# Kernel tuning notes

Hardware: AMD Instinct MI355X
Metric: run time of the kernel (lower is better)

Reference implementation:

```python
import jax, jax.numpy as jnp
import numpy as np

N_HEADS = 12
C = 3          # per-head in/hidden/out channels (12/4)
C_PRED = 1     # predictor hidden (4/4)
BN_EPS = 1e-5
COS_EPS = 1e-8
B, H, W = 8, 512, 768


def setup_inputs() -> dict:
    key = jax.random.key(0)
    ks = jax.random.split(key, 22)
    p = lambda k, s: jax.random.normal(k, s, jnp.float32) * 0.1
    return {
        "latent1": jax.random.normal(ks[0], (B, N_HEADS, H, W), jnp.float32),
        "latent2": jax.random.normal(ks[1], (B, N_HEADS, H, W), jnp.float32),
        # projector conv1 + BN
        "W1": p(ks[2], (N_HEADS, C, C)), "b1": p(ks[3], (N_HEADS, C)),
        "g1": 1.0 + p(ks[4], (N_HEADS, C)), "be1": p(ks[5], (N_HEADS, C)),
        # projector conv2 + BN
        "W2": p(ks[6], (N_HEADS, C, C)), "b2": p(ks[7], (N_HEADS, C)),
        "g2": 1.0 + p(ks[8], (N_HEADS, C)), "be2": p(ks[9], (N_HEADS, C)),
        # projector conv3 + BN (no ReLU)
        "W3": p(ks[10], (N_HEADS, C, C)), "b3": p(ks[11], (N_HEADS, C)),
        "g3": 1.0 + p(ks[12], (N_HEADS, C)), "be3": p(ks[13], (N_HEADS, C)),
        # predictor conv1 + BN
        "W4": p(ks[14], (N_HEADS, C_PRED, C)), "b4": p(ks[15], (N_HEADS, C_PRED)),
        "g4": 1.0 + p(ks[16], (N_HEADS, C_PRED)), "be4": p(ks[17], (N_HEADS, C_PRED)),
        # predictor conv2 (no BN)
        "W5": p(ks[18], (N_HEADS, C, C_PRED)), "b5": p(ks[19], (N_HEADS, C)),
    }


def _conv1x1(x, Wk, bk):
    # x: [B, Cin, H, W'], Wk: [Cout, Cin]
    return jnp.einsum('oc,bchw->bohw', Wk, x) + bk[None, :, None, None]


def _bn(x, g, be):
    # training-mode BatchNorm2d: batch statistics over (B, H, W)
    m = x.mean(axis=(0, 2, 3), keepdims=True)
    v = x.var(axis=(0, 2, 3), keepdims=True)  # biased var, as torch BN uses
    return (x - m) * jax.lax.rsqrt(v + BN_EPS) * g[None, :, None, None] + be[None, :, None, None]


def _cos_loss(p, z):
    # -mean(cosine_similarity(p, detach(z), dim=1))
    z = jax.lax.stop_gradient(z)
    dot = jnp.sum(p * z, axis=1)
    npn = jnp.maximum(jnp.sqrt(jnp.sum(p * p, axis=1)), COS_EPS)
    nzn = jnp.maximum(jnp.sqrt(jnp.sum(z * z, axis=1)), COS_EPS)
    return -jnp.mean(dot / (npn * nzn))


def _head_loss(x1, x2, W1, b1, g1, be1, W2, b2, g2, be2, W3, b3, g3, be3,
               W4, b4, g4, be4, W5, b5):
    def proj(x):
        x = jax.nn.relu(_bn(_conv1x1(x, W1, b1), g1, be1))
        x = jax.nn.relu(_bn(_conv1x1(x, W2, b2), g2, be2))
        return _bn(_conv1x1(x, W3, b3), g3, be3)

    def pred(z):
        h = jax.nn.relu(_bn(_conv1x1(z, W4, b4), g4, be4))
        return _conv1x1(h, W5, b5)

    z1, z2 = proj(x1), proj(x2)
    p1, p2 = pred(z1), pred(z2)
    return 0.5 * (_cos_loss(p1, z2) + _cos_loss(p2, z1))


def reference(latent1, latent2, W1, b1, g1, be1, W2, b2, g2, be2,
              W3, b3, g3, be3, W4, b4, g4, be4, W5, b5):
    Bd, Cd, Hd, Wd = latent1.shape
    Wp = Wd // C
    # per-channel view [B, H, W] -> [B, 3, H, W/3]; stack heads on leading axis
    x1 = latent1.reshape(Bd, N_HEADS, C, Hd, Wp).transpose(1, 0, 2, 3, 4)
    x2 = latent2.reshape(Bd, N_HEADS, C, Hd, Wp).transpose(1, 0, 2, 3, 4)
    losses = jax.vmap(_head_loss)(x1, x2, W1, b1, g1, be1, W2, b2, g2, be2,
                                  W3, b3, g3, be3, W4, b4, g4, be4, W5, b5)
    return jnp.sum(losses)
```

## Files before the change

kernel.cpp:

```cpp
#include <hip/hip_runtime.h>
#include <math.h>


typedef unsigned short ushort_t;
typedef unsigned int uint_t;

constexpr int   NH      = 12;
constexpr int   POS     = 131072;
constexpr int   NB      = 8;
constexpr long long MLL = (long long)NB * POS;
constexpr int   CSPAN   = POS / 16;
constexpr int   SBLK    = 128;
constexpr int   NTOT    = NB * NH * 3 * POS;
constexpr float COS_EPS = 1e-8f;

constexpr size_t XB_BYTES   = (size_t)NTOT * 2;
constexpr size_t DBL_COUNT  = (size_t)24 * SBLK * 9 + (size_t)24 * SBLK * 6 +
                              (size_t)24 * SBLK * 9 + (size_t)12 * SBLK;
constexpr size_t NEED_BYTES = 2 * XB_BYTES + DBL_COUNT * 8 + 480 * 4;

template <int K>
__device__ inline void block_reduce_to0(double (&v)[K]) {
#pragma unroll
  for (int off = 32; off > 0; off >>= 1) {
#pragma unroll
    for (int k = 0; k < K; ++k) v[k] += __shfl_down(v[k], off, 64);
  }
  __shared__ double lds[4][K];
  const int lane = threadIdx.x & 63;
  const int wv   = threadIdx.x >> 6;
  if (lane == 0) {
#pragma unroll
    for (int k = 0; k < K; ++k) lds[wv][k] = v[k];
  }
  __syncthreads();
  if (threadIdx.x == 0) {
#pragma unroll
    for (int k = 0; k < K; ++k) v[k] = lds[0][k] + lds[1][k] + lds[2][k] + lds[3][k];
  }
}

__device__ inline uint_t pack2bf(float lo, float hi) {
  uint_t ul = __float_as_uint(lo);
  uint_t uh = __float_as_uint(hi);
  ul = ul + 0x7FFFu + ((ul >> 16) & 1u);
  uh = uh + 0x7FFFu + ((uh >> 16) & 1u);
  return (ul >> 16) | (uh & 0xFFFF0000u);
}

__device__ inline void unpack8(const uint4 v, float (&f)[8]) {
  const uint_t w0 = v.x, w1 = v.y, w2 = v.z, w3 = v.w;
  f[0] = __uint_as_float(w0 << 16); f[1] = __uint_as_float(w0 & 0xFFFF0000u);
  f[2] = __uint_as_float(w1 << 16); f[3] = __uint_as_float(w1 & 0xFFFF0000u);
  f[4] = __uint_as_float(w2 << 16); f[5] = __uint_as_float(w2 & 0xFFFF0000u);
  f[6] = __uint_as_float(w3 << 16); f[7] = __uint_as_float(w3 & 0xFFFF0000u);
}

template <bool BF16>
__device__ inline void load_ch3(const float* __restrict__ X,
                                const ushort_t* __restrict__ XB,
                                size_t eoff, float (&f)[3][8]) {
#pragma unroll
  for (int c = 0; c < 3; ++c) {
    const size_t a = eoff + (size_t)c * POS;
    if constexpr (BF16) {
      const uint4 v = *(const uint4*)(XB + a);
      unpack8(v, f[c]);
    } else {
      const float4 u0 = *(const float4*)(X + a);
      const float4 u1 = *(const float4*)(X + a + 4);
      f[c][0] = u0.x; f[c][1] = u0.y; f[c][2] = u0.z; f[c][3] = u0.w;
      f[c][4] = u1.x; f[c][5] = u1.y; f[c][6] = u1.z; f[c][7] = u1.w;
    }
  }
}

template <bool STORE>
__global__ __launch_bounds__(256) void passA_kernel(
    const float* __restrict__ x1, const float* __restrict__ x2,
    ushort_t* __restrict__ xb1, ushort_t* __restrict__ xb2,
    double* __restrict__ P0) {
  const int u = blockIdx.y;
  const int s = u % 24;
  const int b = u / 24;
  const int n = s >> 1;
  const float* __restrict__ X = (s & 1) ? x2 : x1;
  ushort_t* __restrict__ XB = (s & 1) ? xb2 : xb1;
  const size_t off0 = (size_t)((b * NH + n) * 3) * POS + (size_t)blockIdx.x * CSPAN;

  float acc[9] = {0.f, 0.f, 0.f, 0.f, 0.f, 0.f, 0.f, 0.f, 0.f};
#pragma unroll
  for (int i = 0; i < 8; ++i) {
    const int idx = i * 1024 + threadIdx.x * 4;
    float4 v[3];
#pragma unroll
    for (int c = 0; c < 3; ++c)
      v[c] = *(const float4*)(X + off0 + (size_t)c * POS + idx);
    if constexpr (STORE) {
#pragma unroll
      for (int c = 0; c < 3; ++c) {
        uint2 h;
        h.x = pack2bf(v[c].x, v[c].y);
        h.y = pack2bf(v[c].z, v[c].w);
        *(uint2*)(XB + off0 + (size_t)c * POS + idx) = h;
      }
    }
    const float* f0 = (const float*)&v[0];
    const float* f1 = (const float*)&v[1];
    const float* f2 = (const float*)&v[2];
#pragma unroll
    for (int j = 0; j < 4; ++j) {
      const float X0 = f0[j], X1 = f1[j], X2 = f2[j];
      acc[0] += X0;      acc[1] += X1;      acc[2] += X2;
      acc[3] += X0 * X0; acc[4] += X1 * X1; acc[5] += X2 * X2;
      acc[6] += X0 * X1; acc[7] += X0 * X2; acc[8] += X1 * X2;
    }
  }

  double v9[9];
#pragma unroll
  for (int k = 0; k < 9; ++k) v9[k] = (double)acc[k];
  block_reduce_to0<9>(v9);
  if (threadIdx.x == 0) {
    double* dst = P0 + ((size_t)s * SBLK + b * 16 + blockIdx.x) * 9;
#pragma unroll
    for (int k = 0; k < 9; ++k) dst[k] = v9[k];
  }
}

__global__ __launch_bounds__(256) void bn_statsA_kernel(
    const double* __restrict__ P0, const float* __restrict__ W1,
    const float* __restrict__ b1, const float* __restrict__ g1,
    const float* __restrict__ be1, float* __restrict__ derived) {
  const int s = blockIdx.x;
  const int t = threadIdx.x;
  const int n = s >> 1;
  double v[9] = {0, 0, 0, 0, 0, 0, 0, 0, 0};
  if (t < SBLK) {
    const double* p = P0 + ((size_t)s * SBLK + t) * 9;
#pragma unroll
    for (int k = 0; k < 9; ++k) v[k] = p[k];
  }
  block_reduce_to0<9>(v);
  if (t == 0) {
    const double M = (double)MLL;
    double m[3] = {v[0] / M, v[1] / M, v[2] / M};
    double C00 = v[3] / M - m[0] * m[0];
    double C11 = v[4] / M - m[1] * m[1];
    double C22 = v[5] / M - m[2] * m[2];
    double C01 = v[6] / M - m[0] * m[1];
    double C02 = v[7] / M - m[0] * m[2];
    double C12 = v[8] / M - m[1] * m[2];
    for (int o = 0; o < 3; ++o) {
      const double w0 = W1[n * 9 + o * 3 + 0];
      const double w1v = W1[n * 9 + o * 3 + 1];
      const double w2v = W1[n * 9 + o * 3 + 2];
      const double my = w0 * m[0] + w1v * m[1] + w2v * m[2] + (double)b1[n * 3 + o];
      const double vy = w0 * w0 * C00 + w1v * w1v * C11 + w2v * w2v * C22 +
                        2.0 * (w0 * w1v * C01 + w0 * w2v * C02 + w1v * w2v * C12);
      const double sc = (double)g1[n * 3 + o] / sqrt(vy + 1e-5);
      derived[s * 20 + o]     = (float)sc;
      derived[s * 20 + 3 + o] = (float)((double)be1[n * 3 + o] - my * sc);
    }
  }
}

template <bool BF16>
__global__ __launch_bounds__(256) void passB_kernel(
    const float* __restrict__ x1, const float* __restrict__ x2,
    const ushort_t* __restrict__ xb1, const ushort_t* __restrict__ xb2,
    const float* __restrict__ W1, const float* __restrict__ b1,
    const float* __restrict__ W2, const float* __restrict__ b2,
    const float* __restrict__ derived, double* __restrict__ P2) {
  const int u = blockIdx.y;
  const int s = u % 24;
  const int b = u / 24;
  const int n = s >> 1;
  const float* __restrict__ X = (s & 1) ? x2 : x1;
  const ushort_t* __restrict__ XB = (s & 1) ? xb2 : xb1;
  const size_t off0 = (size_t)((b * NH + n) * 3) * POS + (size_t)blockIdx.x * CSPAN;

  float w1[3][3], bb1[3], w2[3][3], bb2[3], s1[3], t1[3];
#pragma unroll
  for (int o = 0; o < 3; ++o) {
#pragma unroll
    for (int c = 0; c < 3; ++c) {
      w1[o][c] = W1[n * 9 + o * 3 + c];
      w2[o][c] = W2[n * 9 + o * 3 + c];
    }
    bb1[o] = b1[n * 3 + o];
    bb2[o] = b2[n * 3 + o];
    s1[o]  = derived[s * 20 + o];
    t1[o]  = derived[s * 20 + 3 + o];
  }

  float acc[6] = {0.f, 0.f, 0.f, 0.f, 0.f, 0.f};
#pragma unroll 2
  for (int i = 0; i < 4; ++i) {
    const size_t eoff = off0 + i * 2048 + threadIdx.x * 8;
    float f[3][8];
    load_ch3<BF16>(X, XB, eoff, f);
#pragma unroll
    for (int j = 0; j < 8; ++j) {
      const float X0 = f[0][j], X1 = f[1][j], X2 = f[2][j];
      float a[3];
#pragma unroll
      for (int o = 0; o < 3; ++o) {
        const float y = fmaf(w1[o][0], X0, fmaf(w1[o][1], X1, fmaf(w1[o][2], X2, bb1[o])));
        a[o] = fmaxf(0.f, fmaf(s1[o], y, t1[o]));
      }
#pragma unroll
      for (int o = 0; o < 3; ++o) {
        const float y2v = fmaf(w2[o][0], a[0], fmaf(w2[o][1], a[1], fmaf(w2[o][2], a[2], bb2[o])));
        acc[o]     += y2v;
        acc[3 + o] += y2v * y2v;
      }
    }
  }

  double v[6];
#pragma unroll
  for (int k = 0; k < 6; ++k) v[k] = (double)acc[k];
  block_reduce_to0<6>(v);
  if (threadIdx.x == 0) {
    double* dst = P2 + ((size_t)s * SBLK + b * 16 + blockIdx.x) * 6;
#pragma unroll
    for (int k = 0; k < 6; ++k) dst[k] = v[k];
  }
}

__global__ __launch_bounds__(256) void bn_statsB_kernel(
    const double* __restrict__ P2, const float* __restrict__ gamma,
    const float* __restrict__ beta, float* __restrict__ derived) {
  const int s = blockIdx.x;
  const int t = threadIdx.x;
  const int n = s >> 1;
  double v[6] = {0, 0, 0, 0, 0, 0};
  if (t < SBLK) {
    const double* p = P2 + ((size_t)s * SBLK + t) * 6;
#pragma unroll
    for (int k = 0; k < 6; ++k) v[k] = p[k];
  }
  block_reduce_to0<6>(v);
  if (t == 0) {
#pragma unroll
    for (int c = 0; c < 3; ++c) {
      const double mean = v[c] / (double)MLL;
      const double var  = v[3 + c] / (double)MLL - mean * mean;
      const double sc   = (double)gamma[n * 3 + c] / sqrt(var + 1e-5);
      derived[s * 20 + 6 + c] = (float)sc;
      derived[s * 20 + 9 + c] = (float)((double)beta[n * 3 + c] - mean * sc);
    }
  }
}

template <bool BF16>
__global__ __launch_bounds__(256) void passC_kernel(
    const float* __restrict__ x1, const float* __restrict__ x2,
    const ushort_t* __restrict__ xb1, const ushort_t* __restrict__ xb2,
    const float* __restrict__ W1, const float* __restrict__ b1,
    const float* __restrict__ W2, const float* __restrict__ b2,
    const float* __restrict__ W3, const float* __restrict__ b3,
    const float* __restrict__ derived, double* __restrict__ P3) {
  const int u = blockIdx.y;
  const int s = u % 24;
  const int b = u / 24;
  const int n = s >> 1;
  const float* __restrict__ X = (s & 1) ? x2 : x1;
  const ushort_t* __restrict__ XB = (s & 1) ? xb2 : xb1;
  const size_t off0 = (size_t)((b * NH + n) * 3) * POS + (size_t)blockIdx.x * CSPAN;

  float w1[3][3], bb1[3], w2[3][3], bb2[3], w3[3][3], bb3[3];
  float s1[3], t1[3], s2[3], t2[3];
#pragma unroll
  for (int o = 0; o < 3; ++o) {
#pragma unroll
    for (int c = 0; c < 3; ++c) {
      w1[o][c] = W1[n * 9 + o * 3 + c];
      w2[o][c] = W2[n * 9 + o * 3 + c];
      w3[o][c] = W3[n * 9 + o * 3 + c];
    }
    bb1[o] = b1[n * 3 + o];
    bb2[o] = b2[n * 3 + o];
    bb3[o] = b3[n * 3 + o];
    s1[o]  = derived[s * 20 + o];
    t1[o]  = derived[s * 20 + 3 + o];
    s2[o]  = derived[s * 20 + 6 + o];
    t2[o]  = derived[s * 20 + 9 + o];
  }

  float acc[9] = {0.f, 0.f, 0.f, 0.f, 0.f, 0.f, 0.f, 0.f, 0.f};
#pragma unroll 2
  for (int i = 0; i < 4; ++i) {
    const size_t eoff = off0 + i * 2048 + threadIdx.x * 8;
    float f[3][8];
    load_ch3<BF16>(X, XB, eoff, f);
#pragma unroll
    for (int j = 0; j < 8; ++j) {
      const float X0 = f[0][j], X1 = f[1][j], X2 = f[2][j];
      float a[3], a2[3], y3[3];
#pragma unroll
      for (int o = 0; o < 3; ++o) {
        const float y = fmaf(w1[o][0], X0, fmaf(w1[o][1], X1, fmaf(w1[o][2], X2, bb1[o])));
        a[o] = fmaxf(0.f, fmaf(s1[o], y, t1[o]));
      }
#pragma unroll
      for (int o = 0; o < 3; ++o) {
        const float y = fmaf(w2[o][0], a[0], fmaf(w2[o][1], a[1], fmaf(w2[o][2], a[2], bb2[o])));
        a2[o] = fmaxf(0.f, fmaf(s2[o], y, t2[o]));
      }
#pragma unroll
      for (int o = 0; o < 3; ++o) {
        y3[o] = fmaf(w3[o][0], a2[0], fmaf(w3[o][1], a2[1], fmaf(w3[o][2], a2[2], bb3[o])));
        acc[o]     += y3[o];
        acc[3 + o] += y3[o] * y3[o];
      }
      acc[6] += y3[0] * y3[1];
      acc[7] += y3[0] * y3[2];
      acc[8] += y3[1] * y3[2];
    }
  }

  double v[9];
#pragma unroll
  for (int k = 0; k < 9; ++k) v[k] = (double)acc[k];
  block_reduce_to0<9>(v);
  if (threadIdx.x == 0) {
    double* dst = P3 + ((size_t)s * SBLK + b * 16 + blockIdx.x) * 9;
#pragma unroll
    for (int k = 0; k < 9; ++k) dst[k] = v[k];
  }
}

__global__ __launch_bounds__(256) void bn_statsC_kernel(
    const double* __restrict__ P3, const float* __restrict__ g3,
    const float* __restrict__ be3, const float* __restrict__ W4,
    const float* __restrict__ b4, const float* __restrict__ g4,
    const float* __restrict__ be4, float* __restrict__ derived) {
  const int s = blockIdx.x;
  const int t = threadIdx.x;
  const int n = s >> 1;
  double v[9] = {0, 0, 0, 0, 0, 0, 0, 0, 0};
  if (t < SBLK) {
    const double* p = P3 + ((size_t)s * SBLK + t) * 9;
#pragma unroll
    for (int k = 0; k < 9; ++k) v[k] = p[k];
  }
  block_reduce_to0<9>(v);
  if (t == 0) {
    const double M = (double)MLL;
    double mean[3] = {v[0] / M, v[1] / M, v[2] / M};
    double cov[3][3];
    cov[0][0] = v[3] / M - mean[0] * mean[0];
    cov[1][1] = v[4] / M - mean[1] * mean[1];
    cov[2][2] = v[5] / M - mean[2] * mean[2];
    cov[0][1] = cov[1][0] = v[6] / M - mean[0] * mean[1];
    cov[0][2] = cov[2][0] = v[7] / M - mean[0] * mean[2];
    cov[1][2] = cov[2][1] = v[8] / M - mean[1] * mean[2];

    double s3[3], t3[3];
    for (int c = 0; c < 3; ++c) {
      s3[c] = (double)g3[n * 3 + c] / sqrt(cov[c][c] + 1e-5);
      t3[c] = (double)be3[n * 3 + c] - mean[c] * s3[c];
      derived[s * 20 + 12 + c] = (float)s3[c];
      derived[s * 20 + 15 + c] = (float)t3[c];
    }
    double u[3], dd = (double)b4[n];
    for (int c = 0; c < 3; ++c) {
      u[c] = (double)W4[n * 3 + c] * s3[c];
      dd += (double)W4[n * 3 + c] * t3[c];
    }
    double m4 = dd;
    for (int c = 0; c < 3; ++c) m4 += u[c] * mean[c];
    double v4 = 0.0;
    for (int i = 0; i < 3; ++i)
      for (int j = 0; j < 3; ++j) v4 += u[i] * u[j] * cov[i][j];
    const double s4 = (double)g4[n] / sqrt(v4 + 1e-5);
    derived[s * 20 + 18] = (float)s4;
    derived[s * 20 + 19] = (float)((double)be4[n] - m4 * s4);
  }
}

__device__ inline void fwd_chain(
    const float w1[3][3], const float bb1[3],
    const float w2[3][3], const float bb2[3],
    const float w3[3][3], const float bb3[3],
    const float w4[3], float b4s, const float w5[3], const float b5v[3],
    const float* S, float X0, float X1, float X2, float z[3], float p[3]) {
  float a[3], a2[3];
#pragma unroll
  for (int o = 0; o < 3; ++o) {
    const float y = fmaf(w1[o][0], X0, fmaf(w1[o][1], X1, fmaf(w1[o][2], X2, bb1[o])));
    a[o] = fmaxf(0.f, fmaf(S[o], y, S[3 + o]));
  }
#pragma unroll
  for (int o = 0; o < 3; ++o) {
    const float y = fmaf(w2[o][0], a[0], fmaf(w2[o][1], a[1], fmaf(w2[o][2], a[2], bb2[o])));
    a2[o] = fmaxf(0.f, fmaf(S[6 + o], y, S[9 + o]));
  }
  float y4 = b4s;
#pragma unroll
  for (int o = 0; o < 3; ++o) {
    const float y = fmaf(w3[o][0], a2[0], fmaf(w3[o][1], a2[1], fmaf(w3[o][2], a2[2], bb3[o])));
    z[o] = fmaf(S[12 + o], y, S[15 + o]);
    y4 = fmaf(w4[o], z[o], y4);
  }
  const float h = fmaxf(0.f, fmaf(S[18], y4, S[19]));
#pragma unroll
  for (int o = 0; o < 3; ++o) p[o] = fmaf(w5[o], h, b5v[o]);
}

template <bool BF16>
__global__ __launch_bounds__(256) void passD_kernel(
    const float* __restrict__ x1, const float* __restrict__ x2,
    const ushort_t* __restrict__ xb1, const ushort_t* __restrict__ xb2,
    const float* __restrict__ W1, const float* __restrict__ b1,
    const float* __restrict__ W2, const float* __restrict__ b2,
    const float* __restrict__ W3, const float* __restrict__ b3,
    const float* __restrict__ W4, const float* __restrict__ b4,
    const float* __restrict__ W5, const float* __restrict__ b5,
    const float* __restrict__ derived, double* __restrict__ PL) {
  const int u = blockIdx.y;
  const int n = u % 12;
  const int b = u / 12;
  const size_t off0 = (size_t)((b * NH + n) * 3) * POS + (size_t)blockIdx.x * CSPAN;

  float w1[3][3], bb1[3], w2[3][3], bb2[3], w3[3][3], bb3[3];
  float w4[3], b4s, w5[3], b5v[3];
#pragma unroll
  for (int o = 0; o < 3; ++o) {
#pragma unroll
    for (int c = 0; c < 3; ++c) {
      w1[o][c] = W1[n * 9 + o * 3 + c];
      w2[o][c] = W2[n * 9 + o * 3 + c];
      w3[o][c] = W3[n * 9 + o * 3 + c];
    }
    bb1[o] = b1[n * 3 + o];
    bb2[o] = b2[n * 3 + o];
    bb3[o] = b3[n * 3 + o];
    w4[o]  = W4[n * 3 + o];
    w5[o]  = W5[n * 3 + o];
    b5v[o] = b5[n * 3 + o];
  }
  b4s = b4[n];

  float S0[20], S1[20];
#pragma unroll
  for (int k = 0; k < 20; ++k) {
    S0[k] = derived[(n * 2 + 0) * 20 + k];
    S1[k] = derived[(n * 2 + 1) * 20 + k];
  }

  float acc = 0.f;
  for (int i = 0; i < 4; ++i) {
    const size_t eoff = off0 + i * 2048 + threadIdx.x * 8;
    float fA[3][8], fB[3][8];
    load_ch3<BF16>(x1, xb1, eoff, fA);
    load_ch3<BF16>(x2, xb2, eoff, fB);
#pragma unroll
    for (int j = 0; j < 8; ++j) {
      float z1[3], p1[3], z2[3], p2[3];
      fwd_chain(w1, bb1, w2, bb2, w3, bb3, w4, b4s, w5, b5v, S0,
                fA[0][j], fA[1][j], fA[2][j], z1, p1);
      fwd_chain(w1, bb1, w2, bb2, w3, bb3, w4, b4s, w5, b5v, S1,
                fB[0][j], fB[1][j], fB[2][j], z2, p2);

      const float d12 = p1[0] * z2[0] + p1[1] * z2[1] + p1[2] * z2[2];
      const float pp1 = p1[0] * p1[0] + p1[1] * p1[1] + p1[2] * p1[2];
      const float zz2 = z2[0] * z2[0] + z2[1] * z2[1] + z2[2] * z2[2];
      const float c12 = d12 / (fmaxf(sqrtf(pp1), COS_EPS) * fmaxf(sqrtf(zz2), COS_EPS));

      const float d21 = p2[0] * z1[0] + p2[1] * z1[1] + p2[2] * z1[2];
      const float pp2 = p2[0] * p2[0] + p2[1] * p2[1] + p2[2] * p2[2];
      const float zz1 = z1[0] * z1[0] + z1[1] * z1[1] + z1[2] * z1[2];
      const float c21 = d21 / (fmaxf(sqrtf(pp2), COS_EPS) * fmaxf(sqrtf(zz1), COS_EPS));

      acc += c12 + c21;
    }
  }

  double v[1] = {(double)acc};
  block_reduce_to0<1>(v);
  if (threadIdx.x == 0) PL[(size_t)n * SBLK + b * 16 + blockIdx.x] = v[0];
}

__global__ __launch_bounds__(256) void finalize_kernel(
    const double* __restrict__ PL, float* __restrict__ out) {
  double v[1] = {0.0};
  for (int k = threadIdx.x; k < 12 * SBLK; k += 256) v[0] += PL[k];
  block_reduce_to0<1>(v);
  if (threadIdx.x == 0) out[0] = (float)(-0.5 * v[0] / (double)MLL);
}

extern "C" void kernel_launch(void* const* d_in, const int* in_sizes, int n_in,
                              void* d_out, int out_size, void* d_ws, size_t ws_size,
                              hipStream_t stream) {
  const float* x1  = (const float*)d_in[0];
  const float* x2  = (const float*)d_in[1];
  const float* W1  = (const float*)d_in[2];
  const float* b1  = (const float*)d_in[3];
  const float* g1  = (const float*)d_in[4];
  const float* be1 = (const float*)d_in[5];
  const float* W2  = (const float*)d_in[6];
  const float* b2  = (const float*)d_in[7];
  const float* g2  = (const float*)d_in[8];
  const float* be2 = (const float*)d_in[9];
  const float* W3  = (const float*)d_in[10];
  const float* b3  = (const float*)d_in[11];
  const float* g3  = (const float*)d_in[12];
  const float* be3 = (const float*)d_in[13];
  const float* W4  = (const float*)d_in[14];
  const float* b4  = (const float*)d_in[15];
  const float* g4  = (const float*)d_in[16];
  const float* be4 = (const float*)d_in[17];
  const float* W5  = (const float*)d_in[18];
  const float* b5  = (const float*)d_in[19];

  const bool big = ws_size >= NEED_BYTES;
  ushort_t* xb1 = nullptr;
  ushort_t* xb2 = nullptr;
  double* dbase;
  if (big) {
    xb1 = (ushort_t*)d_ws;
    xb2 = xb1 + NTOT;
    dbase = (double*)(xb2 + NTOT);
  } else {
    dbase = (double*)d_ws;
  }
  double* P0 = dbase;
  double* P2 = P0 + (size_t)24 * SBLK * 9;
  double* P3 = P2 + (size_t)24 * SBLK * 6;
  double* PL = P3 + (size_t)24 * SBLK * 9;
  float* derived = (float*)(PL + 12 * SBLK);

  const dim3 blk(256);
  const dim3 gA(16, 192);
  const dim3 gD(16, 96);

  if (big) {
    passA_kernel<true><<<gA, blk, 0, stream>>>(x1, x2, xb1, xb2, P0);
    bn_statsA_kernel<<<24, blk, 0, stream>>>(P0, W1, b1, g1, be1, derived);
    passB_kernel<true><<<gA, blk, 0, stream>>>(x1, x2, xb1, xb2, W1, b1, W2, b2,
                                               derived, P2);
    bn_statsB_kernel<<<24, blk, 0, stream>>>(P2, g2, be2, derived);
    passC_kernel<true><<<gA, blk, 0, stream>>>(x1, x2, xb1, xb2, W1, b1, W2, b2,
                                               W3, b3, derived, P3);
    bn_statsC_kernel<<<24, blk, 0, stream>>>(P3, g3, be3, W4, b4, g4, be4, derived);
    passD_kernel<true><<<gD, blk, 0, stream>>>(x1, x2, xb1, xb2, W1, b1, W2, b2,
                                               W3, b3, W4, b4, W5, b5, derived, PL);
  } else {
    passA_kernel<false><<<gA, blk, 0, stream>>>(x1, x2, nullptr, nullptr, P0);
    bn_statsA_kernel<<<24, blk, 0, stream>>>(P0, W1, b1, g1, be1, derived);
    passB_kernel<false><<<gA, blk, 0, stream>>>(x1, x2, nullptr, nullptr, W1, b1,
                                                W2, b2, derived, P2);
    bn_statsB_kernel<<<24, blk, 0, stream>>>(P2, g2, be2, derived);
    passC_kernel<false><<<gA, blk, 0, stream>>>(x1, x2, nullptr, nullptr, W1, b1,
                                                W2, b2, W3, b3, derived, P3);
    bn_statsC_kernel<<<24, blk, 0, stream>>>(P3, g3, be3, W4, b4, g4, be4, derived);
    passD_kernel<false><<<gD, blk, 0, stream>>>(x1, x2, nullptr, nullptr, W1, b1,
                                                W2, b2, W3, b3, W4, b4, W5, b5,
                                                derived, PL);
  }
  finalize_kernel<<<1, blk, 0, stream>>>(PL, (float*)d_out);
}
```

Baseline: 515.4 us.

## Materialize layer activations in fp16 workspace and fold BN into conv weights

Each pass now stores its post-ReLU activations back into a half-precision workspace buffer, overwriting the previous layer's values. The next pass reads them directly instead of recomputing the whole projector chain from the input. BatchNorm scale and shift are folded into the conv weights and biases in the stats kernels, so each layer becomes a single affine map plus ReLU. The cosine divide is replaced with rsq intrinsics. In exchange, each pass writes an extra fp16 tensor, and fp16 storage of intermediates brings range and precision risk compared with the earlier bf16 copy of the raw input.

New measurement: 505.8 us. No clear change (-1.9%).

```diff
diff --git a/kernel.cpp b/kernel.cpp
--- a/kernel.cpp
+++ b/kernel.cpp
@@ -1,9 +1,10 @@
 #include <hip/hip_runtime.h>
+#include <hip/hip_fp16.h>
 #include <math.h>
 
 
 typedef unsigned short ushort_t;
-typedef unsigned int uint_t;
+typedef unsigned int   uint_t;
 
 constexpr int   NH      = 12;
 constexpr int   POS     = 131072;
@@ -12,12 +13,11 @@
 constexpr int   CSPAN   = POS / 16;
 constexpr int   SBLK    = 128;
 constexpr int   NTOT    = NB * NH * 3 * POS;
-constexpr float COS_EPS = 1e-8f;
-
-constexpr size_t XB_BYTES   = (size_t)NTOT * 2;
-constexpr size_t DBL_COUNT  = (size_t)24 * SBLK * 9 + (size_t)24 * SBLK * 6 +
-                              (size_t)24 * SBLK * 9 + (size_t)12 * SBLK;
-constexpr size_t NEED_BYTES = 2 * XB_BYTES + DBL_COUNT * 8 + 480 * 4;
+
+constexpr size_t XH_BYTES   = (size_t)NTOT * 2;
+constexpr size_t P_CNT      = (size_t)24 * SBLK * 9;
+constexpr size_t DBL_COUNT  = 3 * P_CNT + (size_t)12 * SBLK;
+constexpr size_t NEED_BYTES = 2 * XH_BYTES + DBL_COUNT * 8 + (size_t)24 * 40 * 4;
 
 template <int K>
 __device__ inline void block_reduce_to0(double (&v)[K]) {
@@ -40,32 +40,30 @@
   }
 }
 
-__device__ inline uint_t pack2bf(float lo, float hi) {
-  uint_t ul = __float_as_uint(lo);
-  uint_t uh = __float_as_uint(hi);
-  ul = ul + 0x7FFFu + ((ul >> 16) & 1u);
-  uh = uh + 0x7FFFu + ((uh >> 16) & 1u);
-  return (ul >> 16) | (uh & 0xFFFF0000u);
-}
-
-__device__ inline void unpack8(const uint4 v, float (&f)[8]) {
-  const uint_t w0 = v.x, w1 = v.y, w2 = v.z, w3 = v.w;
-  f[0] = __uint_as_float(w0 << 16); f[1] = __uint_as_float(w0 & 0xFFFF0000u);
-  f[2] = __uint_as_float(w1 << 16); f[3] = __uint_as_float(w1 & 0xFFFF0000u);
-  f[4] = __uint_as_float(w2 << 16); f[5] = __uint_as_float(w2 & 0xFFFF0000u);
-  f[6] = __uint_as_float(w3 << 16); f[7] = __uint_as_float(w3 & 0xFFFF0000u);
-}
-
-template <bool BF16>
-__device__ inline void load_ch3(const float* __restrict__ X,
-                                const ushort_t* __restrict__ XB,
-                                size_t eoff, float (&f)[3][8]) {
+__device__ inline uint_t pack2h(float lo, float hi) {
+  return (uint_t)__half_as_ushort(__float2half(lo)) |
+         ((uint_t)__half_as_ushort(__float2half(hi)) << 16);
+}
+__device__ inline float h_lo(uint_t w) {
+  return __half2float(__ushort_as_half((unsigned short)(w & 0xFFFFu)));
+}
+__device__ inline float h_hi(uint_t w) {
+  return __half2float(__ushort_as_half((unsigned short)(w >> 16)));
+}
+
+template <bool H16>
+__device__ inline void load3x8(const float* __restrict__ X,
+                               const ushort_t* __restrict__ XH,
+                               size_t e, float (&f)[3][8]) {
 #pragma unroll
   for (int c = 0; c < 3; ++c) {
-    const size_t a = eoff + (size_t)c * POS;
-    if constexpr (BF16) {
-      const uint4 v = *(const uint4*)(XB + a);
-      unpack8(v, f[c]);
+    const size_t a = e + (size_t)c * POS;
+    if constexpr (H16) {
+      const uint4 v = *(const uint4*)(XH + a);
+      f[c][0] = h_lo(v.x); f[c][1] = h_hi(v.x);
+      f[c][2] = h_lo(v.y); f[c][3] = h_hi(v.y);
+      f[c][4] = h_lo(v.z); f[c][5] = h_hi(v.z);
+      f[c][6] = h_lo(v.w); f[c][7] = h_hi(v.w);
     } else {
       const float4 u0 = *(const float4*)(X + a);
       const float4 u1 = *(const float4*)(X + a + 4);
@@ -75,42 +73,42 @@
   }
 }
 
+__device__ inline void store8h(ushort_t* __restrict__ XH, size_t e,
+                               const float (&g)[8]) {
+  uint4 h;
+  h.x = pack2h(g[0], g[1]);
+  h.y = pack2h(g[2], g[3]);
+  h.z = pack2h(g[4], g[5]);
+  h.w = pack2h(g[6], g[7]);
+  *(uint4*)(XH + e) = h;
+}
+
 template <bool STORE>
-__global__ __launch_bounds__(256) void passA_kernel(
+__global__ __launch_bounds__(256) void passA1_kernel(
     const float* __restrict__ x1, const float* __restrict__ x2,
-    ushort_t* __restrict__ xb1, ushort_t* __restrict__ xb2,
+    ushort_t* __restrict__ xh1, ushort_t* __restrict__ xh2,
     double* __restrict__ P0) {
   const int u = blockIdx.y;
   const int s = u % 24;
   const int b = u / 24;
   const int n = s >> 1;
   const float* __restrict__ X = (s & 1) ? x2 : x1;
-  ushort_t* __restrict__ XB = (s & 1) ? xb2 : xb1;
+  ushort_t* __restrict__ XH = (s & 1) ? xh2 : xh1;
   const size_t off0 = (size_t)((b * NH + n) * 3) * POS + (size_t)blockIdx.x * CSPAN;
 
   float acc[9] = {0.f, 0.f, 0.f, 0.f, 0.f, 0.f, 0.f, 0.f, 0.f};
-#pragma unroll
-  for (int i = 0; i < 8; ++i) {
-    const int idx = i * 1024 + threadIdx.x * 4;
-    float4 v[3];
-#pragma unroll
-    for (int c = 0; c < 3; ++c)
-      v[c] = *(const float4*)(X + off0 + (size_t)c * POS + idx);
+#pragma unroll 2
+  for (int i = 0; i < 4; ++i) {
+    const size_t e = off0 + i * 2048 + threadIdx.x * 8;
+    float f[3][8];
+    load3x8<false>(X, nullptr, e, f);
     if constexpr (STORE) {
 #pragma unroll
-      for (int c = 0; c < 3; ++c) {
-        uint2 h;
-        h.x = pack2bf(v[c].x, v[c].y);
-        h.y = pack2bf(v[c].z, v[c].w);
-        *(uint2*)(XB + off0 + (size_t)c * POS + idx) = h;
-      }
-    }
-    const float* f0 = (const float*)&v[0];
-    const float* f1 = (const float*)&v[1];
-    const float* f2 = (const float*)&v[2];
-#pragma unroll
-    for (int j = 0; j < 4; ++j) {
-      const float X0 = f0[j], X1 = f1[j], X2 = f2[j];
+      for (int c = 0; c < 3; ++c) store8h(XH, e + (size_t)c * POS, f[c]);
+    }
+#pragma unroll
+    for (int j = 0; j < 8; ++j) {
+      const float X0 = f[0][j], X1 = f[1][j], X2 = f[2][j];
       acc[0] += X0;      acc[1] += X1;      acc[2] += X2;
       acc[3] += X0 * X0; acc[4] += X1 * X1; acc[5] += X2 * X2;
       acc[6] += X0 * X1; acc[7] += X0 * X2; acc[8] += X1 * X2;
@@ -128,212 +126,188 @@
   }
 }
 
-__global__ __launch_bounds__(256) void bn_statsA_kernel(
-    const double* __restrict__ P0, const float* __restrict__ W1,
-    const float* __restrict__ b1, const float* __restrict__ g1,
-    const float* __restrict__ be1, float* __restrict__ derived) {
+__device__ inline void moments_to_mc(const double (&v)[9], double (&m)[3],
+                                     double (&C)[3][3]) {
+  const double M = (double)MLL;
+  m[0] = v[0] / M; m[1] = v[1] / M; m[2] = v[2] / M;
+  C[0][0] = v[3] / M - m[0] * m[0];
+  C[1][1] = v[4] / M - m[1] * m[1];
+  C[2][2] = v[5] / M - m[2] * m[2];
+  C[0][1] = C[1][0] = v[6] / M - m[0] * m[1];
+  C[0][2] = C[2][0] = v[7] / M - m[0] * m[2];
+  C[1][2] = C[2][1] = v[8] / M - m[1] * m[2];
+}
+
+__global__ __launch_bounds__(256) void stats_fold_kernel(
+    const double* __restrict__ P, const float* __restrict__ Wk,
+    const float* __restrict__ bk, const float* __restrict__ gk,
+    const float* __restrict__ bek, float* __restrict__ derived, int outoff) {
   const int s = blockIdx.x;
   const int t = threadIdx.x;
   const int n = s >> 1;
   double v[9] = {0, 0, 0, 0, 0, 0, 0, 0, 0};
   if (t < SBLK) {
-    const double* p = P0 + ((size_t)s * SBLK + t) * 9;
+    const double* p = P + ((size_t)s * SBLK + t) * 9;
 #pragma unroll
     for (int k = 0; k < 9; ++k) v[k] = p[k];
   }
   block_reduce_to0<9>(v);
   if (t == 0) {
-    const double M = (double)MLL;
-    double m[3] = {v[0] / M, v[1] / M, v[2] / M};
-    double C00 = v[3] / M - m[0] * m[0];
-    double C11 = v[4] / M - m[1] * m[1];
-    double C22 = v[5] / M - m[2] * m[2];
-    double C01 = v[6] / M - m[0] * m[1];
-    double C02 = v[7] / M - m[0] * m[2];
-    double C12 = v[8] / M - m[1] * m[2];
+    double m[3], C[3][3];
+    moments_to_mc(v, m, C);
     for (int o = 0; o < 3; ++o) {
-      const double w0 = W1[n * 9 + o * 3 + 0];
-      const double w1v = W1[n * 9 + o * 3 + 1];
-      const double w2v = W1[n * 9 + o * 3 + 2];
-      const double my = w0 * m[0] + w1v * m[1] + w2v * m[2] + (double)b1[n * 3 + o];
-      const double vy = w0 * w0 * C00 + w1v * w1v * C11 + w2v * w2v * C22 +
-                        2.0 * (w0 * w1v * C01 + w0 * w2v * C02 + w1v * w2v * C12);
-      const double sc = (double)g1[n * 3 + o] / sqrt(vy + 1e-5);
-      derived[s * 20 + o]     = (float)sc;
-      derived[s * 20 + 3 + o] = (float)((double)be1[n * 3 + o] - my * sc);
-    }
-  }
-}
-
-template <bool BF16>
-__global__ __launch_bounds__(256) void passB_kernel(
+      const double w0 = Wk[n * 9 + o * 3 + 0];
+      const double w1 = Wk[n * 9 + o * 3 + 1];
+      const double w2 = Wk[n * 9 + o * 3 + 2];
+      const double my = w0 * m[0] + w1 * m[1] + w2 * m[2] + (double)bk[n * 3 + o];
+      const double vy = w0 * w0 * C[0][0] + w1 * w1 * C[1][1] + w2 * w2 * C[2][2] +
+                        2.0 * (w0 * w1 * C[0][1] + w0 * w2 * C[0][2] + w1 * w2 * C[1][2]);
+      const double sc = (double)gk[n * 3 + o] / sqrt(vy + 1e-5);
+      const double tt = (double)bek[n * 3 + o] - my * sc;
+      derived[s * 40 + outoff + o * 3 + 0] = (float)(sc * w0);
+      derived[s * 40 + outoff + o * 3 + 1] = (float)(sc * w1);
+      derived[s * 40 + outoff + o * 3 + 2] = (float)(sc * w2);
+      derived[s * 40 + outoff + 9 + o]     = (float)(sc * (double)bk[n * 3 + o] + tt);
+    }
+  }
+}
+
+template <bool H16>
+__global__ __launch_bounds__(256) void passA2_kernel(
     const float* __restrict__ x1, const float* __restrict__ x2,
-    const ushort_t* __restrict__ xb1, const ushort_t* __restrict__ xb2,
-    const float* __restrict__ W1, const float* __restrict__ b1,
-    const float* __restrict__ W2, const float* __restrict__ b2,
+    ushort_t* __restrict__ xh1, ushort_t* __restrict__ xh2,
+    const float* __restrict__ derived, double* __restrict__ P1) {
+  const int u = blockIdx.y;
+  const int s = u % 24;
+  const int b = u / 24;
+  const int n = s >> 1;
+  const float* __restrict__ X = (s & 1) ? x2 : x1;
+  ushort_t* __restrict__ XH = (s & 1) ? xh2 : xh1;
+  const size_t off0 = (size_t)((b * NH + n) * 3) * POS + (size_t)blockIdx.x * CSPAN;
+
+  const float* D = derived + s * 40;
+  float w1f[3][3], c1v[3];
+#pragma unroll
+  for (int o = 0; o < 3; ++o) {
+#pragma unroll
+    for (int c = 0; c < 3; ++c) w1f[o][c] = D[o * 3 + c];
+    c1v[o] = D[9 + o];
+  }
+
+  float acc[9] = {0.f, 0.f, 0.f, 0.f, 0.f, 0.f, 0.f, 0.f, 0.f};
+#pragma unroll 2
+  for (int i = 0; i < 4; ++i) {
+    const size_t e = off0 + i * 2048 + threadIdx.x * 8;
+    float f[3][8];
+    load3x8<H16>(X, XH, e, f);
+    float A[3][8];
+#pragma unroll
+    for (int j = 0; j < 8; ++j) {
+      const float X0 = f[0][j], X1 = f[1][j], X2 = f[2][j];
+#pragma unroll
+      for (int o = 0; o < 3; ++o)
+        A[o][j] = fmaxf(0.f, fmaf(w1f[o][0], X0,
+                         fmaf(w1f[o][1], X1, fmaf(w1f[o][2], X2, c1v[o]))));
+      const float A0 = A[0][j], A1 = A[1][j], A2v = A[2][j];
+      acc[0] += A0;       acc[1] += A1;       acc[2] += A2v;
+      acc[3] += A0 * A0;  acc[4] += A1 * A1;  acc[5] += A2v * A2v;
+      acc[6] += A0 * A1;  acc[7] += A0 * A2v; acc[8] += A1 * A2v;
+    }
+    if constexpr (H16) {
+#pragma unroll
+      for (int c = 0; c < 3; ++c) store8h(XH, e + (size_t)c * POS, A[c]);
+    }
+  }
+
+  double v9[9];
+#pragma unroll
+  for (int k = 0; k < 9; ++k) v9[k] = (double)acc[k];
+  block_reduce_to0<9>(v9);
+  if (threadIdx.x == 0) {
+    double* dst = P1 + ((size_t)s * SBLK + b * 16 + blockIdx.x) * 9;
+#pragma unroll
+    for (int k = 0; k < 9; ++k) dst[k] = v9[k];
+  }
+}
+
+template <bool H16>
+__global__ __launch_bounds__(256) void passC2_kernel(
+    const float* __restrict__ x1, const float* __restrict__ x2,
+    ushort_t* __restrict__ xh1, ushort_t* __restrict__ xh2,
     const float* __restrict__ derived, double* __restrict__ P2) {
   const int u = blockIdx.y;
   const int s = u % 24;
   const int b = u / 24;
   const int n = s >> 1;
   const float* __restrict__ X = (s & 1) ? x2 : x1;
-  const ushort_t* __restrict__ XB = (s & 1) ? xb2 : xb1;
+  ushort_t* __restrict__ XH = (s & 1) ? xh2 : xh1;
   const size_t off0 = (size_t)((b * NH + n) * 3) * POS + (size_t)blockIdx.x * CSPAN;
 
-  float w1[3][3], bb1[3], w2[3][3], bb2[3], s1[3], t1[3];
+  const float* D = derived + s * 40;
+  float w1f[3][3], c1v[3];
+  if constexpr (!H16) {
+#pragma unroll
+    for (int o = 0; o < 3; ++o) {
+#pragma unroll
+      for (int c = 0; c < 3; ++c) w1f[o][c] = D[o * 3 + c];
+      c1v[o] = D[9 + o];
+    }
+  }
+  float w2f[3][3], c2v[3];
 #pragma unroll
   for (int o = 0; o < 3; ++o) {
 #pragma unroll
-    for (int c = 0; c < 3; ++c) {
-      w1[o][c] = W1[n * 9 + o * 3 + c];
-      w2[o][c] = W2[n * 9 + o * 3 + c];
-    }
-    bb1[o] = b1[n * 3 + o];
-    bb2[o] = b2[n * 3 + o];
-    s1[o]  = derived[s * 20 + o];
-    t1[o]  = derived[s * 20 + 3 + o];
-  }
-
-  float acc[6] = {0.f, 0.f, 0.f, 0.f, 0.f, 0.f};
-#pragma unroll 2
-  for (int i = 0; i < 4; ++i) {
-    const size_t eoff = off0 + i * 2048 + threadIdx.x * 8;
-    float f[3][8];
-    load_ch3<BF16>(X, XB, eoff, f);
-#pragma unroll
-    for (int j = 0; j < 8; ++j) {
-      const float X0 = f[0][j], X1 = f[1][j], X2 = f[2][j];
-      float a[3];
-#pragma unroll
-      for (int o = 0; o < 3; ++o) {
-        const float y = fmaf(w1[o][0], X0, fmaf(w1[o][1], X1, fmaf(w1[o][2], X2, bb1[o])));
-        a[o] = fmaxf(0.f, fmaf(s1[o], y, t1[o]));
-      }
-#pragma unroll
-      for (int o = 0; o < 3; ++o) {
-        const float y2v = fmaf(w2[o][0], a[0], fmaf(w2[o][1], a[1], fmaf(w2[o][2], a[2], bb2[o])));
-        acc[o]     += y2v;
-        acc[3 + o] += y2v * y2v;
-      }
-    }
-  }
-
-  double v[6];
-#pragma unroll
-  for (int k = 0; k < 6; ++k) v[k] = (double)acc[k];
-  block_reduce_to0<6>(v);
-  if (threadIdx.x == 0) {
-    double* dst = P2 + ((size_t)s * SBLK + b * 16 + blockIdx.x) * 6;
-#pragma unroll
-    for (int k = 0; k < 6; ++k) dst[k] = v[k];
-  }
-}
-
-__global__ __launch_bounds__(256) void bn_statsB_kernel(
-    const double* __restrict__ P2, const float* __restrict__ gamma,
-    const float* __restrict__ beta, float* __restrict__ derived) {
-  const int s = blockIdx.x;
-  const int t = threadIdx.x;
-  const int n = s >> 1;
-  double v[6] = {0, 0, 0, 0, 0, 0};
-  if (t < SBLK) {
-    const double* p = P2 + ((size_t)s * SBLK + t) * 6;
-#pragma unroll
-    for (int k = 0; k < 6; ++k) v[k] = p[k];
-  }
-  block_reduce_to0<6>(v);
-  if (t == 0) {
-#pragma unroll
-    for (int c = 0; c < 3; ++c) {
-      const double mean = v[c] / (double)MLL;
-      const double var  = v[3 + c] / (double)MLL - mean * mean;
-      const double sc   = (double)gamma[n * 3 + c] / sqrt(var + 1e-5);
-      derived[s * 20 + 6 + c] = (float)sc;
-      derived[s * 20 + 9 + c] = (float)((double)beta[n * 3 + c] - mean * sc);
-    }
-  }
-}
-
-template <bool BF16>
-__global__ __launch_bounds__(256) void passC_kernel(
-    const float* __restrict__ x1, const float* __restrict__ x2,
-    const ushort_t* __restrict__ xb1, const ushort_t* __restrict__ xb2,
-    const float* __restrict__ W1, const float* __restrict__ b1,
-    const float* __restrict__ W2, const float* __restrict__ b2,
-    const float* __restrict__ W3, const float* __restrict__ b3,
-    const float* __restrict__ derived, double* __restrict__ P3) {
-  const int u = blockIdx.y;
-  const int s = u % 24;
-  const int b = u / 24;
-  const int n = s >> 1;
-  const float* __restrict__ X = (s & 1) ? x2 : x1;
-  const ushort_t* __restrict__ XB = (s & 1) ? xb2 : xb1;
-  const size_t off0 = (size_t)((b * NH + n) * 3) * POS + (size_t)blockIdx.x * CSPAN;
-
-  float w1[3][3], bb1[3], w2[3][3], bb2[3], w3[3][3], bb3[3];
-  float s1[3], t1[3], s2[3], t2[3];
-#pragma unroll
-  for (int o = 0; o < 3; ++o) {
-#pragma unroll
-    for (int c = 0; c < 3; ++c) {
-      w1[o][c] = W1[n * 9 + o * 3 + c];
-      w2[o][c] = W2[n * 9 + o * 3 + c];
-      w3[o][c] = W3[n * 9 + o * 3 + c];
-    }
-    bb1[o] = b1[n * 3 + o];
-    bb2[o] = b2[n * 3 + o];
-    bb3[o] = b3[n * 3 + o];
-    s1[o]  = derived[s * 20 + o];
-    t1[o]  = derived[s * 20 + 3 + o];
-    s2[o]  = derived[s * 20 + 6 + o];
-    t2[o]  = derived[s * 20 + 9 + o];
+    for (int c = 0; c < 3; ++c) w2f[o][c] = D[12 + o * 3 + c];
+    c2v[o] = D[21 + o];
   }
 
   float acc[9] = {0.f, 0.f, 0.f, 0.f, 0.f, 0.f, 0.f, 0.f, 0.f};
 #pragma unroll 2
   for (int i = 0; i < 4; ++i) {
-    const size_t eoff = off0 + i * 2048 + threadIdx.x * 8;
+    const size_t e = off0 + i * 2048 + threadIdx.x * 8;
     float f[3][8];
-    load_ch3<BF16>(X, XB, eoff, f);
+    load3x8<H16>(X, XH, e, f);
+    float A[3][8];
 #pragma unroll
     for (int j = 0; j < 8; ++j) {
-      const float X0 = f[0][j], X1 = f[1][j], X2 = f[2][j];
-      float a[3], a2[3], y3[3];
-#pragma unroll
-      for (int o = 0; o < 3; ++o) {
-        const float y = fmaf(w1[o][0], X0, fmaf(w1[o][1], X1, fmaf(w1[o][2], X2, bb1[o])));
-        a[o] = fmaxf(0.f, fmaf(s1[o], y, t1[o]));
+      float a0, a1, a2;
+      if constexpr (H16) {
+        a0 = f[0][j]; a1 = f[1][j]; a2 = f[2][j];
+      } else {
+        const float X0 = f[0][j], X1 = f[1][j], X2 = f[2][j];
+        a0 = fmaxf(0.f, fmaf(w1f[0][0], X0, fmaf(w1f[0][1], X1, fmaf(w1f[0][2], X2, c1v[0]))));
+        a1 = fmaxf(0.f, fmaf(w1f[1][0], X0, fmaf(w1f[1][1], X1, fmaf(w1f[1][2], X2, c1v[1]))));
+        a2 = fmaxf(0.f, fmaf(w1f[2][0], X0, fmaf(w1f[2][1], X1, fmaf(w1f[2][2], X2, c1v[2]))));
       }
 #pragma unroll
-      for (int o = 0; o < 3; ++o) {
-        const float y = fmaf(w2[o][0], a[0], fmaf(w2[o][1], a[1], fmaf(w2[o][2], a[2], bb2[o])));
-        a2[o] = fmaxf(0.f, fmaf(s2[o], y, t2[o]));
-      }
-#pragma unroll
-      for (int o = 0; o < 3; ++o) {
-        y3[o] = fmaf(w3[o][0], a2[0], fmaf(w3[o][1], a2[1], fmaf(w3[o][2], a2[2], bb3[o])));
-        acc[o]     += y3[o];
-        acc[3 + o] += y3[o] * y3[o];
-      }
-      acc[6] += y3[0] * y3[1];
-      acc[7] += y3[0] * y3[2];
-      acc[8] += y3[1] * y3[2];
-    }
-  }
-
-  double v[9];
-#pragma unroll
-  for (int k = 0; k < 9; ++k) v[k] = (double)acc[k];
-  block_reduce_to0<9>(v);
+      for (int o = 0; o < 3; ++o)
+        A[o][j] = fmaxf(0.f, fmaf(w2f[o][0], a0,
+                         fmaf(w2f[o][1], a1, fmaf(w2f[o][2], a2, c2v[o]))));
+      const float A0 = A[0][j], A1 = A[1][j], A2v = A[2][j];
+      acc[0] += A0;       acc[1] += A1;       acc[2] += A2v;
+      acc[3] += A0 * A0;  acc[4] += A1 * A1;  acc[5] += A2v * A2v;
+      acc[6] += A0 * A1;  acc[7] += A0 * A2v; acc[8] += A1 * A2v;
+    }
+    if constexpr (H16) {
+#pragma unroll
+      for (int c = 0; c < 3; ++c) store8h(XH, e + (size_t)c * POS, A[c]);
+    }
+  }
+
+  double v9[9];
+#pragma unroll
+  for (int k = 0; k < 9; ++k) v9[k] = (double)acc[k];
+  block_reduce_to0<9>(v9);
   if (threadIdx.x == 0) {
-    double* dst = P3 + ((size_t)s * SBLK + b * 16 + blockIdx.x) * 9;
-#pragma unroll
-    for (int k = 0; k < 9; ++k) dst[k] = v[k];
-  }
-}
-
-__global__ __launch_bounds__(256) void bn_statsC_kernel(
-    const double* __restrict__ P3, const float* __restrict__ g3,
+    double* dst = P2 + ((size_t)s * SBLK + b * 16 + blockIdx.x) * 9;
+#pragma unroll
+    for (int k = 0; k < 9; ++k) dst[k] = v9[k];
+  }
+}
+
+__global__ __launch_bounds__(256) void statsC2_kernel(
+    const double* __restrict__ P2, const float* __restrict__ W3,
+    const float* __restrict__ b3, const float* __restrict__ g3,
     const float* __restrict__ be3, const float* __restrict__ W4,
     const float* __restrict__ b4, const float* __restrict__ g4,
     const float* __restrict__ be4, float* __restrict__ derived) {
@@ -342,82 +316,82 @@
   const int n = s >> 1;
   double v[9] = {0, 0, 0, 0, 0, 0, 0, 0, 0};
   if (t < SBLK) {
-    const double* p = P3 + ((size_t)s * SBLK + t) * 9;
+    const double* p = P2 + ((size_t)s * SBLK + t) * 9;
 #pragma unroll
     for (int k = 0; k < 9; ++k) v[k] = p[k];
   }
   block_reduce_to0<9>(v);
   if (t == 0) {
-    const double M = (double)MLL;
-    double mean[3] = {v[0] / M, v[1] / M, v[2] / M};
-    double cov[3][3];
-    cov[0][0] = v[3] / M - mean[0] * mean[0];
-    cov[1][1] = v[4] / M - mean[1] * mean[1];
-    cov[2][2] = v[5] / M - mean[2] * mean[2];
-    cov[0][1] = cov[1][0] = v[6] / M - mean[0] * mean[1];
-    cov[0][2] = cov[2][0] = v[7] / M - mean[0] * mean[2];
-    cov[1][2] = cov[2][1] = v[8] / M - mean[1] * mean[2];
-
-    double s3[3], t3[3];
-    for (int c = 0; c < 3; ++c) {
-      s3[c] = (double)g3[n * 3 + c] / sqrt(cov[c][c] + 1e-5);
-      t3[c] = (double)be3[n * 3 + c] - mean[c] * s3[c];
-      derived[s * 20 + 12 + c] = (float)s3[c];
-      derived[s * 20 + 15 + c] = (float)t3[c];
-    }
-    double u[3], dd = (double)b4[n];
-    for (int c = 0; c < 3; ++c) {
-      u[c] = (double)W4[n * 3 + c] * s3[c];
-      dd += (double)W4[n * 3 + c] * t3[c];
-    }
-    double m4 = dd;
-    for (int c = 0; c < 3; ++c) m4 += u[c] * mean[c];
+    double m[3], C[3][3];
+    moments_to_mc(v, m, C);
+    double F3d[3][3], c3d[3];
+    for (int o = 0; o < 3; ++o) {
+      const double w0 = W3[n * 9 + o * 3 + 0];
+      const double w1 = W3[n * 9 + o * 3 + 1];
+      const double w2 = W3[n * 9 + o * 3 + 2];
+      const double m3 = w0 * m[0] + w1 * m[1] + w2 * m[2] + (double)b3[n * 3 + o];
+      const double vy = w0 * w0 * C[0][0] + w1 * w1 * C[1][1] + w2 * w2 * C[2][2] +
+                        2.0 * (w0 * w1 * C[0][1] + w0 * w2 * C[0][2] + w1 * w2 * C[1][2]);
+      const double s3 = (double)g3[n * 3 + o] / sqrt(vy + 1e-5);
+      const double t3 = (double)be3[n * 3 + o] - m3 * s3;
+      F3d[o][0] = s3 * w0; F3d[o][1] = s3 * w1; F3d[o][2] = s3 * w2;
+      c3d[o] = s3 * (double)b3[n * 3 + o] + t3;
+      derived[s * 40 + 24 + o * 3 + 0] = (float)F3d[o][0];
+      derived[s * 40 + 24 + o * 3 + 1] = (float)F3d[o][1];
+      derived[s * 40 + 24 + o * 3 + 2] = (float)F3d[o][2];
+      derived[s * 40 + 33 + o]         = (float)c3d[o];
+    }
+    double q[3] = {0.0, 0.0, 0.0};
+    double d = (double)b4[n];
+    for (int o = 0; o < 3; ++o) {
+      const double w4o = W4[n * 3 + o];
+      q[0] += w4o * F3d[o][0];
+      q[1] += w4o * F3d[o][1];
+      q[2] += w4o * F3d[o][2];
+      d += w4o * c3d[o];
+    }
+    const double m4 = q[0] * m[0] + q[1] * m[1] + q[2] * m[2] + d;
     double v4 = 0.0;
-    for (int i = 0; i < 3; ++i)
-      for (int j = 0; j < 3; ++j) v4 += u[i] * u[j] * cov[i][j];
+    for (int i2 = 0; i2 < 3; ++i2)
+      for (int j2 = 0; j2 < 3; ++j2) v4 += q[i2] * q[j2] * C[i2][j2];
     const double s4 = (double)g4[n] / sqrt(v4 + 1e-5);
-    derived[s * 20 + 18] = (float)s4;
-    derived[s * 20 + 19] = (float)((double)be4[n] - m4 * s4);
-  }
-}
-
-__device__ inline void fwd_chain(
-    const float w1[3][3], const float bb1[3],
-    const float w2[3][3], const float bb2[3],
-    const float w3[3][3], const float bb3[3],
-    const float w4[3], float b4s, const float w5[3], const float b5v[3],
-    const float* S, float X0, float X1, float X2, float z[3], float p[3]) {
-  float a[3], a2[3];
-#pragma unroll
-  for (int o = 0; o < 3; ++o) {
-    const float y = fmaf(w1[o][0], X0, fmaf(w1[o][1], X1, fmaf(w1[o][2], X2, bb1[o])));
-    a[o] = fmaxf(0.f, fmaf(S[o], y, S[3 + o]));
-  }
-#pragma unroll
-  for (int o = 0; o < 3; ++o) {
-    const float y = fmaf(w2[o][0], a[0], fmaf(w2[o][1], a[1], fmaf(w2[o][2], a[2], bb2[o])));
-    a2[o] = fmaxf(0.f, fmaf(S[6 + o], y, S[9 + o]));
-  }
-  float y4 = b4s;
-#pragma unroll
-  for (int o = 0; o < 3; ++o) {
-    const float y = fmaf(w3[o][0], a2[0], fmaf(w3[o][1], a2[1], fmaf(w3[o][2], a2[2], bb3[o])));
-    z[o] = fmaf(S[12 + o], y, S[15 + o]);
-    y4 = fmaf(w4[o], z[o], y4);
-  }
-  const float h = fmaxf(0.f, fmaf(S[18], y4, S[19]));
+    const double t4 = (double)be4[n] - m4 * s4;
+    for (int o = 0; o < 3; ++o)
+      derived[s * 40 + 36 + o] = (float)(s4 * (double)W4[n * 3 + o]);
+    derived[s * 40 + 39] = (float)(s4 * (double)b4[n] + t4);
+  }
+}
+
+template <bool H16>
+__device__ inline void tail_chain(
+    const float (&F1)[3][3], const float (&C1)[3],
+    const float (&F2)[3][3], const float (&C2)[3],
+    const float (&F3)[3][3], const float (&C3)[3],
+    const float (&W4s)[3], float B4c,
+    const float (&w5)[3], const float (&b5v)[3],
+    float v0, float v1, float v2, float (&z)[3], float (&p)[3]) {
+  float a0 = v0, a1 = v1, a2 = v2;
+  if constexpr (!H16) {
+    const float t0 = fmaxf(0.f, fmaf(F1[0][0], v0, fmaf(F1[0][1], v1, fmaf(F1[0][2], v2, C1[0]))));
+    const float t1 = fmaxf(0.f, fmaf(F1[1][0], v0, fmaf(F1[1][1], v1, fmaf(F1[1][2], v2, C1[1]))));
+    const float t2 = fmaxf(0.f, fmaf(F1[2][0], v0, fmaf(F1[2][1], v1, fmaf(F1[2][2], v2, C1[2]))));
+    a0 = fmaxf(0.f, fmaf(F2[0][0], t0, fmaf(F2[0][1], t1, fmaf(F2[0][2], t2, C2[0]))));
+    a1 = fmaxf(0.f, fmaf(F2[1][0], t0, fmaf(F2[1][1], t1, fmaf(F2[1][2], t2, C2[1]))));
+    a2 = fmaxf(0.f, fmaf(F2[2][0], t0, fmaf(F2[2][1], t1, fmaf(F2[2][2], t2, C2[2]))));
+  }
+#pragma unroll
+  for (int o = 0; o < 3; ++o)
+    z[o] = fmaf(F3[o][0], a0, fmaf(F3[o][1], a1, fmaf(F3[o][2], a2, C3[o])));
+  const float y4 = fmaf(W4s[0], z[0], fmaf(W4s[1], z[1], fmaf(W4s[2], z[2], B4c)));
+  const float h = fmaxf(0.f, y4);
 #pragma unroll
   for (int o = 0; o < 3; ++o) p[o] = fmaf(w5[o], h, b5v[o]);
 }
 
-template <bool BF16>
-__global__ __launch_bounds__(256) void passD_kernel(
+template <bool H16>
+__global__ __launch_bounds__(256) void passD2_kernel(
     const float* __restrict__ x1, const float* __restrict__ x2,
-    const ushort_t* __restrict__ xb1, const ushort_t* __restrict__ xb2,
-    const float* __restrict__ W1, const float* __restrict__ b1,
-    const float* __restrict__ W2, const float* __restrict__ b2,
-    const float* __restrict__ W3, const float* __restrict__ b3,
-    const float* __restrict__ W4, const float* __restrict__ b4,
+    const ushort_t* __restrict__ xh1, const ushort_t* __restrict__ xh2,
     const float* __restrict__ W5, const float* __restrict__ b5,
     const float* __restrict__ derived, double* __restrict__ PL) {
   const int u = blockIdx.y;
@@ -425,57 +399,64 @@
   const int b = u / 12;
   const size_t off0 = (size_t)((b * NH + n) * 3) * POS + (size_t)blockIdx.x * CSPAN;
 
-  float w1[3][3], bb1[3], w2[3][3], bb2[3], w3[3][3], bb3[3];
-  float w4[3], b4s, w5[3], b5v[3];
+  float F1[2][3][3], C1[2][3], F2[2][3][3], C2[2][3];
+  float F3[2][3][3], C3[2][3], W4s[2][3], B4c[2];
+#pragma unroll
+  for (int br = 0; br < 2; ++br) {
+    const float* D = derived + (size_t)(2 * n + br) * 40;
+    if constexpr (!H16) {
+#pragma unroll
+      for (int o = 0; o < 3; ++o) {
+#pragma unroll
+        for (int c = 0; c < 3; ++c) {
+          F1[br][o][c] = D[o * 3 + c];
+          F2[br][o][c] = D[12 + o * 3 + c];
+        }
+        C1[br][o] = D[9 + o];
+        C2[br][o] = D[21 + o];
+      }
+    }
+#pragma unroll
+    for (int o = 0; o < 3; ++o) {
+#pragma unroll
+      for (int c = 0; c < 3; ++c) F3[br][o][c] = D[24 + o * 3 + c];
+      C3[br][o]  = D[33 + o];
+      W4s[br][o] = D[36 + o];
+    }
+    B4c[br] = D[39];
+  }
+  float w5[3], b5v[3];
 #pragma unroll
   for (int o = 0; o < 3; ++o) {
-#pragma unroll
-    for (int c = 0; c < 3; ++c) {
-      w1[o][c] = W1[n * 9 + o * 3 + c];
-      w2[o][c] = W2[n * 9 + o * 3 + c];
-      w3[o][c] = W3[n * 9 + o * 3 + c];
-    }
-    bb1[o] = b1[n * 3 + o];
-    bb2[o] = b2[n * 3 + o];
-    bb3[o] = b3[n * 3 + o];
-    w4[o]  = W4[n * 3 + o];
     w5[o]  = W5[n * 3 + o];
     b5v[o] = b5[n * 3 + o];
   }
-  b4s = b4[n];
-
-  float S0[20], S1[20];
-#pragma unroll
-  for (int k = 0; k < 20; ++k) {
-    S0[k] = derived[(n * 2 + 0) * 20 + k];
-    S1[k] = derived[(n * 2 + 1) * 20 + k];
-  }
 
   float acc = 0.f;
   for (int i = 0; i < 4; ++i) {
-    const size_t eoff = off0 + i * 2048 + threadIdx.x * 8;
+    const size_t e = off0 + i * 2048 + threadIdx.x * 8;
     float fA[3][8], fB[3][8];
-    load_ch3<BF16>(x1, xb1, eoff, fA);
-    load_ch3<BF16>(x2, xb2, eoff, fB);
+    load3x8<H16>(x1, xh1, e, fA);
+    load3x8<H16>(x2, xh2, e, fB);
 #pragma unroll
     for (int j = 0; j < 8; ++j) {
       float z1[3], p1[3], z2[3], p2[3];
-      fwd_chain(w1, bb1, w2, bb2, w3, bb3, w4, b4s, w5, b5v, S0,
-                fA[0][j], fA[1][j], fA[2][j], z1, p1);
-      fwd_chain(w1, bb1, w2, bb2, w3, bb3, w4, b4s, w5, b5v, S1,
-                fB[0][j], fB[1][j], fB[2][j], z2, p2);
+      tail_chain<H16>(F1[0], C1[0], F2[0], C2[0], F3[0], C3[0], W4s[0], B4c[0],
+                      w5, b5v, fA[0][j], fA[1][j], fA[2][j], z1, p1);
+      tail_chain<H16>(F1[1], C1[1], F2[1], C2[1], F3[1], C3[1], W4s[1], B4c[1],
+                      w5, b5v, fB[0][j], fB[1][j], fB[2][j], z2, p2);
 
       const float d12 = p1[0] * z2[0] + p1[1] * z2[1] + p1[2] * z2[2];
       const float pp1 = p1[0] * p1[0] + p1[1] * p1[1] + p1[2] * p1[2];
       const float zz2 = z2[0] * z2[0] + z2[1] * z2[1] + z2[2] * z2[2];
-      const float c12 = d12 / (fmaxf(sqrtf(pp1), COS_EPS) * fmaxf(sqrtf(zz2), COS_EPS));
+      acc += d12 * __builtin_amdgcn_rsqf(fmaxf(pp1, 1e-16f)) *
+                   __builtin_amdgcn_rsqf(fmaxf(zz2, 1e-16f));
 
       const float d21 = p2[0] * z1[0] + p2[1] * z1[1] + p2[2] * z1[2];
       const float pp2 = p2[0] * p2[0] + p2[1] * p2[1] + p2[2] * p2[2];
       const float zz1 = z1[0] * z1[0] + z1[1] * z1[1] + z1[2] * z1[2];
-      const float c21 = d21 / (fmaxf(sqrtf(pp2), COS_EPS) * fmaxf(sqrtf(zz1), COS_EPS));
-
-      acc += c12 + c21;
+      acc += d21 * __builtin_amdgcn_rsqf(fmaxf(pp2, 1e-16f)) *
+                   __builtin_amdgcn_rsqf(fmaxf(zz1, 1e-16f));
     }
   }
 
@@ -517,20 +498,20 @@
   const float* b5  = (const float*)d_in[19];
 
   const bool big = ws_size >= NEED_BYTES;
-  ushort_t* xb1 = nullptr;
-  ushort_t* xb2 = nullptr;
+  ushort_t* xh1 = nullptr;
+  ushort_t* xh2 = nullptr;
   double* dbase;
   if (big) {
-    xb1 = (ushort_t*)d_ws;
-    xb2 = xb1 + NTOT;
-    dbase = (double*)(xb2 + NTOT);
+    xh1 = (ushort_t*)d_ws;
+    xh2 = xh1 + NTOT;
+    dbase = (double*)(xh2 + NTOT);
   } else {
     dbase = (double*)d_ws;
   }
   double* P0 = dbase;
-  double* P2 = P0 + (size_t)24 * SBLK * 9;
-  double* P3 = P2 + (size_t)24 * SBLK * 6;
-  double* PL = P3 + (size_t)24 * SBLK * 9;
+  double* P1 = P0 + P_CNT;
+  double* P2 = P1 + P_CNT;
+  double* PL = P2 + P_CNT;
   float* derived = (float*)(PL + 12 * SBLK);
 
   const dim3 blk(256);
@@ -538,28 +519,27 @@
   const dim3 gD(16, 96);
 
   if (big) {
-    passA_kernel<true><<<gA, blk, 0, stream>>>(x1, x2, xb1, xb2, P0);
-    bn_statsA_kernel<<<24, blk, 0, stream>>>(P0, W1, b1, g1, be1, derived);
-    passB_kernel<true><<<gA, blk, 0, stream>>>(x1, x2, xb1, xb2, W1, b1, W2, b2,
-                                               derived, P2);
-    bn_statsB_kernel<<<24, blk, 0, stream>>>(P2, g2, be2, derived);
-    passC_kernel<true><<<gA, blk, 0, stream>>>(x1, x2, xb1, xb2, W1, b1, W2, b2,
-                                               W3, b3, derived, P3);
-    bn_statsC_kernel<<<24, blk, 0, stream>>>(P3, g3, be3, W4, b4, g4, be4, derived);
-    passD_kernel<true><<<gD, blk, 0, stream>>>(x1, x2, xb1, xb2, W1, b1, W2, b2,
-                                               W3, b3, W4, b4, W5, b5, derived, PL);
+    passA1_kernel<true><<<gA, blk, 0, stream>>>(x1, x2, xh1, xh2, P0);
+    stats_fold_kernel<<<24, blk, 0, stream>>>(P0, W1, b1, g1, be1, derived, 0);
+    passA2_kernel<true><<<gA, blk, 0, stream>>>(x1, x2, xh1, xh2, derived, P1);
+    stats_fold_kernel<<<24, blk, 0, stream>>>(P1, W2, b2, g2, be2, derived, 12);
+    passC2_kernel<true><<<gA, blk, 0, stream>>>(x1, x2, xh1, xh2, derived, P2);
+    statsC2_kernel<<<24, blk, 0, stream>>>(P2, W3, b3, g3, be3, W4, b4, g4, be4,
+                                           derived);
+    passD2_kernel<true><<<gD, blk, 0, stream>>>(x1, x2, xh1, xh2, W5, b5,
+                                                derived, PL);
   } else {
-    passA_kernel<false><<<gA, blk, 0, stream>>>(x1, x2, nullptr, nullptr, P0);
-    bn_statsA_kernel<<<24, blk, 0, stream>>>(P0, W1, b1, g1, be1, derived);
-    passB_kernel<false><<<gA, blk, 0, stream>>>(x1, x2, nullptr, nullptr, W1, b1,
-                                                W2, b2, derived, P2);
-    bn_statsB_kernel<<<24, blk, 0, stream>>>(P2, g2, be2, derived);
-    passC_kernel<false><<<gA, blk, 0, stream>>>(x1, x2, nullptr, nullptr, W1, b1,
-                                                W2, b2, W3, b3, derived, P3);
-    bn_statsC_kernel<<<24, blk, 0, stream>>>(P3, g3, be3, W4, b4, g4, be4, derived);
-    passD_kernel<false><<<gD, blk, 0, stream>>>(x1, x2, nullptr, nullptr, W1, b1,
-                                                W2, b2, W3, b3, W4, b4, W5, b5,
-                                                derived, PL);
+    passA1_kernel<false><<<gA, blk, 0, stream>>>(x1, x2, nullptr, nullptr, P0);
+    stats_fold_kernel<<<24, blk, 0, stream>>>(P0, W1, b1, g1, be1, derived, 0);
+    passA2_kernel<false><<<gA, blk, 0, stream>>>(x1, x2, nullptr, nullptr,
+                                                 derived, P1);
+    stats_fold_kernel<<<24, blk, 0, stream>>>(P1, W2, b2, g2, be2, derived, 12);
+    passC2_kernel<false><<<gA, blk, 0, stream>>>(x1, x2, nullptr, nullptr,
+                                                 derived, P2);
+    statsC2_kernel<<<24, blk, 0, stream>>>(P2, W3, b3, g3, be3, W4, b4, g4, be4,
+                                           derived);
+    passD2_kernel<false><<<gD, blk, 0, stream>>>(x1, x2, nullptr, nullptr, W5, b5,
+                                                 derived, PL);
   }
   finalize_kernel<<<1, blk, 0, stream>>>(PL, (float*)d_out);
 }
```
